# Kernel tuning notes

Hardware: AMD Instinct MI355X
Metric: run time of the kernel (lower is better)

Reference implementation:

```python
import jax, jax.numpy as jnp
import numpy as np

N = 3000          # num_sample (nodes)
N_OMICS = 3000    # input feature dims for both omics
ENC1, ENC2, NZ = 256, 128, 64


def _xavier(key, fan_in, fan_out):
    limit = float(np.sqrt(6.0 / (fan_in + fan_out)))
    return jax.random.uniform(key, (fan_in, fan_out), jnp.float32, -limit, limit)


def setup_inputs() -> dict:
    key = jax.random.key(0)
    ks = jax.random.split(key, 20)
    inp = {
        "omics_1": jax.random.normal(ks[0], (N, N_OMICS), jnp.float32),
        "omics_2": jax.random.normal(ks[1], (N, N_OMICS), jnp.float32),
    }
    # random dense adjacency, row-normalized (as a typical normalized graph operator)
    for i, name in enumerate(["adj_feature_omics1", "adj_feature_omics2",
                              "adj_spatial_omics1", "adj_spatial_omics2"]):
        a = jax.random.uniform(ks[2 + i], (N, N), jnp.float32)
        inp[name] = a / jnp.sum(a, axis=1, keepdims=True)
    # GNNLayer weights for the four GAE encoders (xavier uniform, as in reset_parameters)
    dims = [(N_OMICS, ENC1), (ENC1, ENC2), (ENC2, NZ)]
    kidx = 6
    for enc in ["f1", "f2", "s1", "s2"]:
        for li, (fi, fo) in enumerate(dims, start=1):
            inp[f"w_{enc}_{li}"] = _xavier(ks[kidx], fi, fo)
            kidx += 1
    return inp


def _gae_encoder(x, adj, w1, w2, w3):
    # GNNLayer: support = act(x @ W); out = spmm(adj, support). Dropout is identity (eval).
    z = adj @ jnp.tanh(x @ w1)          # [N, ENC1]
    z = adj @ jnp.tanh(z @ w2)          # [N, ENC2]
    z = adj @ (z @ w3)                  # [N, NZ]  (no activation on layer 3)
    adj_hat = jax.nn.sigmoid(z @ z.T)   # [N, N]
    return z, adj_hat


def reference(omics_1, omics_2,
              adj_feature_omics1, adj_feature_omics2,
              adj_spatial_omics1, adj_spatial_omics2,
              w_f1_1, w_f1_2, w_f1_3,
              w_f2_1, w_f2_2, w_f2_3,
              w_s1_1, w_s1_2, w_s1_3,
              w_s2_1, w_s2_2, w_s2_3):
    _, a1 = _gae_encoder(omics_1, adj_feature_omics1, w_f1_1, w_f1_2, w_f1_3)
    _, a2 = _gae_encoder(omics_2, adj_feature_omics2, w_f2_1, w_f2_2, w_f2_3)
    _, a3 = _gae_encoder(omics_1, adj_spatial_omics1, w_s1_1, w_s1_2, w_s1_3)
    _, a4 = _gae_encoder(omics_2, adj_spatial_omics2, w_s2_1, w_s2_2, w_s2_3)
    # stacked reconstructed adjacencies from the four encoders [4, N, N]
    return jnp.stack([a1, a2, a3, a4], axis=0)
```

## Files before the change

### kernel.cpp

```cpp
#include <hip/hip_runtime.h>
#include <stdint.h>
#include <stddef.h>


typedef __attribute__((ext_vector_type(8))) _Float16 half8;
typedef __attribute__((ext_vector_type(4))) float f32x4;

#define PAD 3072
#define MR  3000
#define SQ_STRIDE ((size_t)PAD * PAD)
#define CAST_BLK 1600
#define WT_BLK   128

static __device__ __forceinline__ void async_cp16(const _Float16* g, _Float16* l) {
    __builtin_amdgcn_global_load_lds((const __attribute__((address_space(1))) void*)g,
                                     (__attribute__((address_space(3))) void*)l, 16, 0, 0);
}

struct PrepArgs {
    const float* csrc[6];  _Float16* cdst[6];
    const float* Wsrc[12]; _Float16* Wdst[3];
};

__global__ __launch_bounds__(256) void prep2(PrepArgs p) {
    __shared__ _Float16 lt[64 * 64];
    const int b = blockIdx.x;
    const int t = threadIdx.x;
    if (b < CAST_BLK) {
        const int UPA = PAD * PAD / 8;
        const int TOT = 6 * UPA;
        for (int base = b * 2048; base < TOT; base += CAST_BLK * 2048) {
            f32x4 v[8][2];
            #pragma unroll
            for (int k = 0; k < 8; ++k) {
                const int u   = base + (k << 8) + t;
                const int arr = u / UPA;
                const int rem = u - arr * UPA;
                const int row = rem / 384;
                const int c0  = (rem - row * 384) * 8;
                if (row < MR && c0 < MR) {
                    const float* sp = p.csrc[arr] + (size_t)row * MR + c0;
                    v[k][0] = __builtin_nontemporal_load((const f32x4*)sp);
                    v[k][1] = __builtin_nontemporal_load((const f32x4*)(sp + 4));
                } else {
                    v[k][0] = (f32x4){0.f, 0.f, 0.f, 0.f};
                    v[k][1] = (f32x4){0.f, 0.f, 0.f, 0.f};
                }
            }
            #pragma unroll
            for (int k = 0; k < 8; ++k) {
                const int u   = base + (k << 8) + t;
                const int arr = u / UPA;
                const int rem = u - arr * UPA;
                const int row = rem / 384;
                const int c0  = (rem - row * 384) * 8;
                half8 h;
                #pragma unroll
                for (int j = 0; j < 4; ++j) {
                    h[j]     = (_Float16)v[k][0][j];
                    h[4 + j] = (_Float16)v[k][1][j];
                }
                *(half8*)(p.cdst[arr] + (size_t)row * PAD + c0) = h;
            }
        }
    } else {
        for (int tile = b - CAST_BLK; tile < 816; tile += WT_BLK) {
            const int enc = tile / 204;
            int rem = tile - enc * 204;
            const float* src; _Float16* dst; int fi, fo, ldk, kt, rt;
            if (rem < 192) {
                src = p.Wsrc[enc * 3 + 0]; dst = p.Wdst[0] + (size_t)enc * 256 * PAD;
                fi = MR; fo = 256; ldk = PAD; kt = rem >> 2; rt = rem & 3;
            } else if (rem < 200) {
                rem -= 192;
                src = p.Wsrc[enc * 3 + 1]; dst = p.Wdst[1] + (size_t)enc * 128 * 256;
                fi = 256; fo = 128; ldk = 256; kt = rem >> 1; rt = rem & 1;
            } else {
                rem -= 200;
                src = p.Wsrc[enc * 3 + 2]; dst = p.Wdst[2] + (size_t)enc * 128 * 128;
                fi = 128; fo = 64; ldk = 128; kt = rem >> 1; rt = rem & 1;
            }
            const int k0 = kt * 64, r0 = rt * 64;
            __syncthreads();
            {
                const int kr = t >> 2, cc = (t & 3) << 4;
                const int gk = k0 + kr;
                const bool kok = gk < fi;
                #pragma unroll
                for (int j = 0; j < 16; ++j) {
                    const int gr = r0 + cc + j;
                    const float v = (kok && gr < fo) ? src[(size_t)gk * fo + gr] : 0.f;
                    lt[(cc + j) * 64 + kr] = (_Float16)v;
                }
            }
            __syncthreads();
            {
                const int rr = t >> 2, kk = (t & 3) << 4;
                half8 a  = *(half8*)&lt[rr * 64 + kk];
                half8 bb = *(half8*)&lt[rr * 64 + kk + 8];
                _Float16* dp = dst + (size_t)(r0 + rr) * ldk + k0 + kk;
                *(half8*)dp = a;
                *(half8*)(dp + 8) = bb;
            }
        }
    }
}

struct GArgs {
    const _Float16* Aall; size_t aStride; int aMask;
    const _Float16* Ball; size_t bStride; int bMask;
    void* Call; size_t cStride;
    int M, Ncols, Kp, lda, ldb, ldc, mBound, nBound;
};

template<int ACT, int OMODE, int S>
__global__ __launch_bounds__(256, 3)
void gemm_bt(GArgs ga)
{
    __shared__ _Float16 smem[16384];

    const int z   = blockIdx.z;
    const int e   = z / S;
    const int ksl = z - e * S;
    const int Kslice = ga.Kp / S;
    const int kbase  = ksl * Kslice;

    const _Float16* A = ga.Aall + (size_t)(e & ga.aMask) * ga.aStride;
    const _Float16* B = ga.Ball + (size_t)(e & ga.bMask) * ga.bStride;

    const int tm = blockIdx.x * 128;
    const int tn = blockIdx.y * 128;
    const int t    = threadIdx.x;
    const int lane = t & 63;
    const int w    = t >> 6;
    const int wm   = (w >> 1) * 64;
    const int wn   = (w & 1) * 64;
    const int lr   = lane & 15;
    const int lg   = lane >> 4;

    const int sr  = t >> 2;
    const int sch = t & 3;

    f32x4 acc[4][4];
    const f32x4 zero = {0.f, 0.f, 0.f, 0.f};
    #pragma unroll
    for (int i = 0; i < 4; ++i)
        #pragma unroll
        for (int j = 0; j < 4; ++j) acc[i][j] = zero;

    const int nht = Kslice >> 5;

    auto STAGE = [&](int ht, int buf) {
        const int k0 = kbase + (ht << 5);
        _Float16* As = smem + buf * 8192;
        _Float16* Bs = As + 4096;
        #pragma unroll
        for (int i = 0; i < 2; ++i) {
            const int row = sr + i * 64;
            const int sc  = sch ^ (row & 3);
            async_cp16(A + (size_t)(tm + row) * ga.lda + k0 + sc * 8,
                       As + (row * 4 + sch) * 8);
        }
        #pragma unroll
        for (int i = 0; i < 2; ++i) {
            const int row = sr + i * 64;
            const int sc  = sch ^ (row & 3);
            async_cp16(B + (size_t)(tn + row) * ga.ldb + k0 + sc * 8,
                       Bs + (row * 4 + sch) * 8);
        }
    };

    STAGE(0, 0);
    __syncthreads();
    for (int h = 0; h < nht; ++h) {
        const int cur = h & 1;
        if (h + 1 < nht) STAGE(h + 1, cur ^ 1);
        const _Float16* As = smem + cur * 8192;
        const _Float16* Bs = As + 4096;
        half8 af[4], bf[4];
        #pragma unroll
        for (int mi = 0; mi < 4; ++mi) {
            const int ra = wm + mi * 16 + lr;
            const int ch = lg ^ (ra & 3);
            af[mi] = *(const half8*)(As + ra * 32 + ch * 8);
        }
        #pragma unroll
        for (int ni = 0; ni < 4; ++ni) {
            const int rb = wn + ni * 16 + lr;
            const int ch = lg ^ (rb & 3);
            bf[ni] = *(const half8*)(Bs + rb * 32 + ch * 8);
        }
        #pragma unroll
        for (int mi = 0; mi < 4; ++mi)
            #pragma unroll
            for (int ni = 0; ni < 4; ++ni)
                acc[mi][ni] = __builtin_amdgcn_mfma_f32_16x16x32_f16(
                    af[mi], bf[ni], acc[mi][ni], 0, 0, 0);
        __syncthreads();
    }

    if (OMODE == 0) {
        _Float16* C = (_Float16*)ga.Call + (size_t)e * ga.cStride;
        #pragma unroll
        for (int mi = 0; mi < 4; ++mi)
            #pragma unroll
            for (int rr = 0; rr < 4; ++rr) {
                const int m = tm + wm + mi * 16 + lg * 4 + rr;
                #pragma unroll
                for (int ni = 0; ni < 4; ++ni) {
                    const int n = tn + wn + ni * 16 + lr;
                    float x = acc[mi][ni][rr];
                    if (ACT) x = tanhf(x);
                    const bool ok = (m < ga.M) && (n < ga.Ncols);
                    C[(size_t)m * ga.ldc + n] = ok ? (_Float16)x : (_Float16)0.f;
                }
            }
    } else if (OMODE == 1) {
        _Float16* Cp = (_Float16*)ga.Call + (size_t)z * ga.cStride;
        _Float16* ep = smem + w * 2048;
        #pragma unroll
        for (int hs = 0; hs < 2; ++hs) {
            __syncthreads();
            #pragma unroll
            for (int mi2 = 0; mi2 < 2; ++mi2)
                #pragma unroll
                for (int ni = 0; ni < 4; ++ni)
                    #pragma unroll
                    for (int rr = 0; rr < 4; ++rr) {
                        const int row = mi2 * 16 + lg * 4 + rr;
                        const int col = ni * 16 + lr;
                        const int sw  = (((row ^ (row >> 2)) & 3) << 4);
                        ep[row * 64 + (col ^ sw)] = (_Float16)acc[hs * 2 + mi2][ni][rr];
                    }
            __syncthreads();
            #pragma unroll
            for (int it = 0; it < 4; ++it) {
                const int row = it * 8 + (lane >> 3);
                const int c0  = (lane & 7) * 8;
                const int sw  = (((row ^ (row >> 2)) & 3) << 4);
                half8 v = *(const half8*)&ep[row * 64 + (c0 ^ sw)];
                const int gm = tm + wm + hs * 32 + row;
                const int gn = tn + wn + c0;
                *(half8*)&Cp[(size_t)gm * ga.ldc + gn] = v;
            }
        }
    } else {
        float* Cp = (float*)ga.Call + (size_t)e * ga.cStride;
        float* ep = (float*)smem + w * 2048;
        #pragma unroll
        for (int hs = 0; hs < 2; ++hs) {
            __syncthreads();
            #pragma unroll
            for (int mi2 = 0; mi2 < 2; ++mi2)
                #pragma unroll
                for (int ni = 0; ni < 4; ++ni)
                    #pragma unroll
                    for (int rr = 0; rr < 4; ++rr) {
                        const int row = mi2 * 16 + lg * 4 + rr;
                        const int col = ni * 16 + lr;
                        const int sw  = (((row ^ (row >> 2)) & 3) << 4);
                        ep[row * 64 + (col ^ sw)] = acc[hs * 2 + mi2][ni][rr];
                    }
            __syncthreads();
            #pragma unroll
            for (int r2 = 0; r2 < 8; ++r2) {
                const int row = r2 * 4 + (lane >> 4);
                const int c4  = (lane & 15) * 4;
                const int sw  = (((row ^ (row >> 2)) & 3) << 4);
                f32x4 v = *(const f32x4*)&ep[row * 64 + (c4 ^ sw)];
                const int gm = tm + wm + hs * 32 + row;
                const int gn = tn + wn + c4;
                if (gm < ga.mBound && gn < ga.nBound) {
                    #pragma unroll
                    for (int j = 0; j < 4; ++j)
                        v[j] = 1.0f / (1.0f + __expf(-v[j]));
                    __builtin_nontemporal_store(v, (f32x4*)&Cp[(size_t)gm * ga.ldc + gn]);
                }
            }
        }
    }
}

template<int ACT, int S>
__global__ __launch_bounds__(256)
void reduce_k(const _Float16* __restrict__ P, _Float16* __restrict__ out, size_t region)
{
    const size_t e    = blockIdx.y;
    const size_t base = (size_t)(blockIdx.x * 256 + threadIdx.x) * 8;
    const _Float16* p0 = P + e * S * region + base;
    float s[8] = {0.f, 0.f, 0.f, 0.f, 0.f, 0.f, 0.f, 0.f};
    #pragma unroll
    for (int si = 0; si < S; ++si) {
        half8 v = *(const half8*)(p0 + (size_t)si * region);
        #pragma unroll
        for (int j = 0; j < 8; ++j) s[j] += (float)v[j];
    }
    half8 h;
    #pragma unroll
    for (int j = 0; j < 8; ++j) {
        float x = s[j];
        if (ACT) x = tanhf(x);
        h[j] = (_Float16)x;
    }
    *(half8*)(out + e * region + base) = h;
}

extern "C" void kernel_launch(void* const* d_in, const int* in_sizes, int n_in,
                              void* d_out, int out_size, void* d_ws, size_t ws_size,
                              hipStream_t stream)
{
    const size_t R1 = 786432;
    const size_t R2 = 393216;

    _Float16* Adj    = (_Float16*)d_out;
    _Float16* Part16 = Adj + 4 * SQ_STRIDE;

    _Float16* hb = (_Float16*)d_ws;
    size_t off = 0;
    auto alloc = [&](size_t elems) { _Float16* p = hb + off; off += elems; return p; };
    _Float16* Xh  = alloc(2 * SQ_STRIDE);
    _Float16* T1  = alloc(4 * R1);
    _Float16* Z1  = alloc(4 * R1);
    _Float16* T2  = alloc(4 * R2);
    _Float16* Z2  = alloc(4 * R2);
    _Float16* T3  = alloc(4 * R2);
    _Float16* Z3  = alloc(4 * R2);
    _Float16* W1t = alloc(4ull * 256 * PAD);
    _Float16* W2t = alloc(4ull * 128 * 256);
    _Float16* W3t = alloc(4ull * 128 * 128);

    PrepArgs pa;
    pa.csrc[0] = (const float*)d_in[0]; pa.cdst[0] = Xh;
    pa.csrc[1] = (const float*)d_in[1]; pa.cdst[1] = Xh + SQ_STRIDE;
    for (int i = 0; i < 4; ++i) {
        pa.csrc[2 + i] = (const float*)d_in[2 + i];
        pa.cdst[2 + i] = Adj + (size_t)i * SQ_STRIDE;
    }
    for (int enc = 0; enc < 4; ++enc)
        for (int li = 0; li < 3; ++li)
            pa.Wsrc[enc * 3 + li] = (const float*)d_in[6 + enc * 3 + li];
    pa.Wdst[0] = W1t; pa.Wdst[1] = W2t; pa.Wdst[2] = W3t;
    prep2<<<dim3(CAST_BLK + WT_BLK, 1, 1), 256, 0, stream>>>(pa);

    const int BIG = 1 << 30;

    GArgs g1 = { W1t, (size_t)256 * PAD, 3, Xh, SQ_STRIDE, 1,
                 Part16, R1, 256, PAD, PAD, PAD, PAD, PAD, BIG, BIG };
    gemm_bt<0, 1, 4><<<dim3(2, 24, 16), 256, 0, stream>>>(g1);
    reduce_k<1, 4><<<dim3(384, 4, 1), 256, 0, stream>>>(Part16, T1, R1);

    GArgs g2 = { Adj, SQ_STRIDE, 3, T1, R1, 3,
                 Part16, R1, PAD, 256, PAD, PAD, PAD, 256, BIG, BIG };
    gemm_bt<0, 1, 4><<<dim3(24, 2, 16), 256, 0, stream>>>(g2);
    reduce_k<0, 4><<<dim3(384, 4, 1), 256, 0, stream>>>(Part16, Z1, R1);

    GArgs g3 = { W2t, (size_t)128 * 256, 3, Z1, R1, 3,
                 T2, R2, 128, PAD, 256, 256, 256, PAD, BIG, BIG };
    gemm_bt<1, 0, 1><<<dim3(1, 24, 4), 256, 0, stream>>>(g3);

    GArgs g4 = { Adj, SQ_STRIDE, 3, T2, R2, 3,
                 Part16, R2, PAD, 128, PAD, PAD, PAD, 128, BIG, BIG };
    gemm_bt<0, 1, 8><<<dim3(24, 1, 32), 256, 0, stream>>>(g4);
    reduce_k<0, 8><<<dim3(192, 4, 1), 256, 0, stream>>>(Part16, Z2, R2);

    GArgs g5 = { W3t, (size_t)128 * 128, 3, Z2, R2, 3,
                 T3, R2, 128, PAD, 128, 128, 128, PAD, BIG, BIG };
    gemm_bt<0, 0, 1><<<dim3(1, 24, 4), 256, 0, stream>>>(g5);

    GArgs g6 = { Adj, SQ_STRIDE, 3, T3, R2, 3,
                 Part16, R2, PAD, 128, PAD, PAD, PAD, 128, BIG, BIG };
    gemm_bt<0, 1, 8><<<dim3(24, 1, 32), 256, 0, stream>>>(g6);
    reduce_k<0, 8><<<dim3(192, 4, 1), 256, 0, stream>>>(Part16, Z3, R2);

    GArgs g7 = { Z3, R2, 3, Z3, R2, 3,
                 d_out, (size_t)MR * MR, MR, MR, 64, 128, 128, MR, MR, MR };
    gemm_bt<0, 2, 1><<<dim3(24, 24, 4), 256, 0, stream>>>(g7);
}
```

Before: 265.9 us.

## Replace split-K with partial reductions by smaller-tile full-K GEMMs

Drops split-K for the big GEMMs along with their fp16 partial buffers and separate reduce kernels. Each GEMM now runs over the full K with templated tile shapes (128x64, 64x128, 64x64) to keep enough blocks in the grid. Tanh moves into the GEMM epilogue. This removes the partial-sum write/read traffic and extra launches, but gives fewer blocks and longer K loops per block. It also changes the cast block count and the occupancy hints.

```diff
diff --git a/kernel.cpp b/kernel.cpp
--- a/kernel.cpp
+++ b/kernel.cpp
@@ -9,7 +9,7 @@
 #define PAD 3072
 #define MR  3000
 #define SQ_STRIDE ((size_t)PAD * PAD)
-#define CAST_BLK 1600
+#define CAST_BLK 1728
 #define WT_BLK   128
 
 static __device__ __forceinline__ void async_cp16(const _Float16* g, _Float16* l) {
@@ -113,60 +113,57 @@
     int M, Ncols, Kp, lda, ldb, ldc, mBound, nBound;
 };
 
-template<int ACT, int OMODE, int S>
-__global__ __launch_bounds__(256, 3)
+template<int ACT, int OMODE, int BM, int BN>
+__global__ __launch_bounds__(256, (BM == 128 && BN == 128) ? 2 : 4)
 void gemm_bt(GArgs ga)
 {
-    __shared__ _Float16 smem[16384];
-
-    const int z   = blockIdx.z;
-    const int e   = z / S;
-    const int ksl = z - e * S;
-    const int Kslice = ga.Kp / S;
-    const int kbase  = ksl * Kslice;
-
+    constexpr int AM  = BM / 32;
+    constexpr int AN  = BN / 32;
+    constexpr int AIT = BM / 64;
+    constexpr int BIT = BN / 64;
+    constexpr int HALF = (BM + BN) * 32;
+    __shared__ _Float16 smem[2 * HALF];
+
+    const int e = blockIdx.z;
     const _Float16* A = ga.Aall + (size_t)(e & ga.aMask) * ga.aStride;
     const _Float16* B = ga.Ball + (size_t)(e & ga.bMask) * ga.bStride;
 
-    const int tm = blockIdx.x * 128;
-    const int tn = blockIdx.y * 128;
+    const int tm = blockIdx.x * BM;
+    const int tn = blockIdx.y * BN;
     const int t    = threadIdx.x;
     const int lane = t & 63;
     const int w    = t >> 6;
-    const int wm   = (w >> 1) * 64;
-    const int wn   = (w & 1) * 64;
+    const int wm   = (w >> 1) * (BM / 2);
+    const int wn   = (w & 1) * (BN / 2);
     const int lr   = lane & 15;
     const int lg   = lane >> 4;
 
-    const int sr  = t >> 2;
-    const int sch = t & 3;
-
-    f32x4 acc[4][4];
+    f32x4 acc[AM][AN];
     const f32x4 zero = {0.f, 0.f, 0.f, 0.f};
     #pragma unroll
-    for (int i = 0; i < 4; ++i)
-        #pragma unroll
-        for (int j = 0; j < 4; ++j) acc[i][j] = zero;
-
-    const int nht = Kslice >> 5;
+    for (int i = 0; i < AM; ++i)
+        #pragma unroll
+        for (int j = 0; j < AN; ++j) acc[i][j] = zero;
+
+    const int nht = ga.Kp >> 5;
 
     auto STAGE = [&](int ht, int buf) {
-        const int k0 = kbase + (ht << 5);
-        _Float16* As = smem + buf * 8192;
-        _Float16* Bs = As + 4096;
-        #pragma unroll
-        for (int i = 0; i < 2; ++i) {
-            const int row = sr + i * 64;
+        const int k0 = ht << 5;
+        _Float16* As = smem + buf * HALF;
+        _Float16* Bs = As + BM * 32;
+        #pragma unroll
+        for (int i = 0; i < AIT; ++i) {
+            const int c = t + i * 256;
+            const int row = c >> 2, sch = c & 3;
             const int sc  = sch ^ (row & 3);
-            async_cp16(A + (size_t)(tm + row) * ga.lda + k0 + sc * 8,
-                       As + (row * 4 + sch) * 8);
-        }
-        #pragma unroll
-        for (int i = 0; i < 2; ++i) {
-            const int row = sr + i * 64;
+            async_cp16(A + (size_t)(tm + row) * ga.lda + k0 + sc * 8, As + c * 8);
+        }
+        #pragma unroll
+        for (int i = 0; i < BIT; ++i) {
+            const int c = t + i * 256;
+            const int row = c >> 2, sch = c & 3;
             const int sc  = sch ^ (row & 3);
-            async_cp16(B + (size_t)(tn + row) * ga.ldb + k0 + sc * 8,
-                       Bs + (row * 4 + sch) * 8);
+            async_cp16(B + (size_t)(tn + row) * ga.ldb + k0 + sc * 8, Bs + c * 8);
         }
     };
 
@@ -175,25 +172,25 @@
     for (int h = 0; h < nht; ++h) {
         const int cur = h & 1;
         if (h + 1 < nht) STAGE(h + 1, cur ^ 1);
-        const _Float16* As = smem + cur * 8192;
-        const _Float16* Bs = As + 4096;
-        half8 af[4], bf[4];
-        #pragma unroll
-        for (int mi = 0; mi < 4; ++mi) {
+        const _Float16* As = smem + cur * HALF;
+        const _Float16* Bs = As + BM * 32;
+        half8 af[AM], bf[AN];
+        #pragma unroll
+        for (int mi = 0; mi < AM; ++mi) {
             const int ra = wm + mi * 16 + lr;
             const int ch = lg ^ (ra & 3);
             af[mi] = *(const half8*)(As + ra * 32 + ch * 8);
         }
         #pragma unroll
-        for (int ni = 0; ni < 4; ++ni) {
+        for (int ni = 0; ni < AN; ++ni) {
             const int rb = wn + ni * 16 + lr;
             const int ch = lg ^ (rb & 3);
             bf[ni] = *(const half8*)(Bs + rb * 32 + ch * 8);
         }
         #pragma unroll
-        for (int mi = 0; mi < 4; ++mi)
-            #pragma unroll
-            for (int ni = 0; ni < 4; ++ni)
+        for (int mi = 0; mi < AM; ++mi)
+            #pragma unroll
+            for (int ni = 0; ni < AN; ++ni)
                 acc[mi][ni] = __builtin_amdgcn_mfma_f32_16x16x32_f16(
                     af[mi], bf[ni], acc[mi][ni], 0, 0, 0);
         __syncthreads();
@@ -202,12 +199,12 @@
     if (OMODE == 0) {
         _Float16* C = (_Float16*)ga.Call + (size_t)e * ga.cStride;
         #pragma unroll
-        for (int mi = 0; mi < 4; ++mi)
+        for (int mi = 0; mi < AM; ++mi)
             #pragma unroll
             for (int rr = 0; rr < 4; ++rr) {
                 const int m = tm + wm + mi * 16 + lg * 4 + rr;
                 #pragma unroll
-                for (int ni = 0; ni < 4; ++ni) {
+                for (int ni = 0; ni < AN; ++ni) {
                     const int n = tn + wn + ni * 16 + lr;
                     float x = acc[mi][ni][rr];
                     if (ACT) x = tanhf(x);
@@ -215,36 +212,8 @@
                     C[(size_t)m * ga.ldc + n] = ok ? (_Float16)x : (_Float16)0.f;
                 }
             }
-    } else if (OMODE == 1) {
-        _Float16* Cp = (_Float16*)ga.Call + (size_t)z * ga.cStride;
-        _Float16* ep = smem + w * 2048;
-        #pragma unroll
-        for (int hs = 0; hs < 2; ++hs) {
-            __syncthreads();
-            #pragma unroll
-            for (int mi2 = 0; mi2 < 2; ++mi2)
-                #pragma unroll
-                for (int ni = 0; ni < 4; ++ni)
-                    #pragma unroll
-                    for (int rr = 0; rr < 4; ++rr) {
-                        const int row = mi2 * 16 + lg * 4 + rr;
-                        const int col = ni * 16 + lr;
-                        const int sw  = (((row ^ (row >> 2)) & 3) << 4);
-                        ep[row * 64 + (col ^ sw)] = (_Float16)acc[hs * 2 + mi2][ni][rr];
-                    }
-            __syncthreads();
-            #pragma unroll
-            for (int it = 0; it < 4; ++it) {
-                const int row = it * 8 + (lane >> 3);
-                const int c0  = (lane & 7) * 8;
-                const int sw  = (((row ^ (row >> 2)) & 3) << 4);
-                half8 v = *(const half8*)&ep[row * 64 + (c0 ^ sw)];
-                const int gm = tm + wm + hs * 32 + row;
-                const int gn = tn + wn + c0;
-                *(half8*)&Cp[(size_t)gm * ga.ldc + gn] = v;
-            }
-        }
     } else {
+        static_assert(OMODE != 2 || (BM == 128 && BN == 128), "OMODE2 is 128x128");
         float* Cp = (float*)ga.Call + (size_t)e * ga.cStride;
         float* ep = (float*)smem + w * 2048;
         #pragma unroll
@@ -281,30 +250,6 @@
     }
 }
 
-template<int ACT, int S>
-__global__ __launch_bounds__(256)
-void reduce_k(const _Float16* __restrict__ P, _Float16* __restrict__ out, size_t region)
-{
-    const size_t e    = blockIdx.y;
-    const size_t base = (size_t)(blockIdx.x * 256 + threadIdx.x) * 8;
-    const _Float16* p0 = P + e * S * region + base;
-    float s[8] = {0.f, 0.f, 0.f, 0.f, 0.f, 0.f, 0.f, 0.f};
-    #pragma unroll
-    for (int si = 0; si < S; ++si) {
-        half8 v = *(const half8*)(p0 + (size_t)si * region);
-        #pragma unroll
-        for (int j = 0; j < 8; ++j) s[j] += (float)v[j];
-    }
-    half8 h;
-    #pragma unroll
-    for (int j = 0; j < 8; ++j) {
-        float x = s[j];
-        if (ACT) x = tanhf(x);
-        h[j] = (_Float16)x;
-    }
-    *(half8*)(out + e * region + base) = h;
-}
-
 extern "C" void kernel_launch(void* const* d_in, const int* in_sizes, int n_in,
                               void* d_out, int out_size, void* d_ws, size_t ws_size,
                               hipStream_t stream)
@@ -312,8 +257,7 @@
     const size_t R1 = 786432;
     const size_t R2 = 393216;
 
-    _Float16* Adj    = (_Float16*)d_out;
-    _Float16* Part16 = Adj + 4 * SQ_STRIDE;
+    _Float16* Adj = (_Float16*)d_out;
 
     _Float16* hb = (_Float16*)d_ws;
     size_t off = 0;
@@ -345,34 +289,30 @@
     const int BIG = 1 << 30;
 
     GArgs g1 = { W1t, (size_t)256 * PAD, 3, Xh, SQ_STRIDE, 1,
-                 Part16, R1, 256, PAD, PAD, PAD, PAD, PAD, BIG, BIG };
-    gemm_bt<0, 1, 4><<<dim3(2, 24, 16), 256, 0, stream>>>(g1);
-    reduce_k<1, 4><<<dim3(384, 4, 1), 256, 0, stream>>>(Part16, T1, R1);
+                 T1, R1, 256, PAD, PAD, PAD, PAD, PAD, BIG, BIG };
+    gemm_bt<1, 0, 128, 64><<<dim3(2, 48, 4), 256, 0, stream>>>(g1);
 
     GArgs g2 = { Adj, SQ_STRIDE, 3, T1, R1, 3,
-                 Part16, R1, PAD, 256, PAD, PAD, PAD, 256, BIG, BIG };
-    gemm_bt<0, 1, 4><<<dim3(24, 2, 16), 256, 0, stream>>>(g2);
-    reduce_k<0, 4><<<dim3(384, 4, 1), 256, 0, stream>>>(Part16, Z1, R1);
+                 Z1, R1, PAD, 256, PAD, PAD, PAD, 256, BIG, BIG };
+    gemm_bt<0, 0, 64, 128><<<dim3(48, 2, 4), 256, 0, stream>>>(g2);
 
     GArgs g3 = { W2t, (size_t)128 * 256, 3, Z1, R1, 3,
                  T2, R2, 128, PAD, 256, 256, 256, PAD, BIG, BIG };
-    gemm_bt<1, 0, 1><<<dim3(1, 24, 4), 256, 0, stream>>>(g3);
+    gemm_bt<1, 0, 128, 64><<<dim3(1, 48, 4), 256, 0, stream>>>(g3);
 
     GArgs g4 = { Adj, SQ_STRIDE, 3, T2, R2, 3,
-                 Part16, R2, PAD, 128, PAD, PAD, PAD, 128, BIG, BIG };
-    gemm_bt<0, 1, 8><<<dim3(24, 1, 32), 256, 0, stream>>>(g4);
-    reduce_k<0, 8><<<dim3(192, 4, 1), 256, 0, stream>>>(Part16, Z2, R2);
+                 Z2, R2, PAD, 128, PAD, PAD, PAD, 128, BIG, BIG };
+    gemm_bt<0, 0, 64, 64><<<dim3(48, 2, 4), 256, 0, stream>>>(g4);
 
     GArgs g5 = { W3t, (size_t)128 * 128, 3, Z2, R2, 3,
                  T3, R2, 128, PAD, 128, 128, 128, PAD, BIG, BIG };
-    gemm_bt<0, 0, 1><<<dim3(1, 24, 4), 256, 0, stream>>>(g5);
+    gemm_bt<0, 0, 128, 64><<<dim3(1, 48, 4), 256, 0, stream>>>(g5);
 
     GArgs g6 = { Adj, SQ_STRIDE, 3, T3, R2, 3,
-                 Part16, R2, PAD, 128, PAD, PAD, PAD, 128, BIG, BIG };
-    gemm_bt<0, 1, 8><<<dim3(24, 1, 32), 256, 0, stream>>>(g6);
-    reduce_k<0, 8><<<dim3(192, 4, 1), 256, 0, stream>>>(Part16, Z3, R2);
+                 Z3, R2, PAD, 128, PAD, PAD, PAD, 128, BIG, BIG };
+    gemm_bt<0, 0, 64, 64><<<dim3(48, 2, 4), 256, 0, stream>>>(g6);
 
     GArgs g7 = { Z3, R2, 3, Z3, R2, 3,
                  d_out, (size_t)MR * MR, MR, MR, 64, 128, 128, MR, MR, MR };
-    gemm_bt<0, 2, 1><<<dim3(24, 24, 4), 256, 0, stream>>>(g7);
+    gemm_bt<0, 2, 128, 128><<<dim3(24, 24, 4), 256, 0, stream>>>(g7);
 }
```

Result: slower. 300.6 us (+13.1%).

## Overlap adjacency fp32-to-fp16 cast with first-layer GEMM main loop

Applied to the files above, without the earlier changes.

Moves the conversion of the four adjacency matrices out of the prep kernel and into the layer-1 X·W1 GEMM. Each K-iteration of that GEMM loads one 8-element chunk of adjacency and stores it as fp16 on the next iteration, so the cast's memory traffic overlaps the GEMM's compute. The prep kernel now only casts the two omics inputs, with fewer blocks. This adds register pressure and extra global traffic inside the GEMM, and it relies on the grid size times iterations exactly covering the four adjacency arrays.

```diff
diff --git a/kernel.cpp b/kernel.cpp
--- a/kernel.cpp
+++ b/kernel.cpp
@@ -9,7 +9,8 @@
 #define PAD 3072
 #define MR  3000
 #define SQ_STRIDE ((size_t)PAD * PAD)
-#define CAST_BLK 1600
+#define UPA (PAD * PAD / 8)
+#define CAST_BLK 576
 #define WT_BLK   128
 
 static __device__ __forceinline__ void async_cp16(const _Float16* g, _Float16* l) {
@@ -18,7 +19,7 @@
 }
 
 struct PrepArgs {
-    const float* csrc[6];  _Float16* cdst[6];
+    const float* csrc[2];  _Float16* cdst[2];
     const float* Wsrc[12]; _Float16* Wdst[3];
 };
 
@@ -27,8 +28,7 @@
     const int b = blockIdx.x;
     const int t = threadIdx.x;
     if (b < CAST_BLK) {
-        const int UPA = PAD * PAD / 8;
-        const int TOT = 6 * UPA;
+        const int TOT = 2 * UPA;
         for (int base = b * 2048; base < TOT; base += CAST_BLK * 2048) {
             f32x4 v[8][2];
             #pragma unroll
@@ -112,10 +112,11 @@
     void* Call; size_t cStride;
     int M, Ncols, Kp, lda, ldb, ldc, mBound, nBound;
 };
-
-template<int ACT, int OMODE, int S>
+struct CastA { const float* src[4]; _Float16* dst; };
+
+template<int ACT, int OMODE, int S, int CAST>
 __global__ __launch_bounds__(256, 3)
-void gemm_bt(GArgs ga)
+void gemm_bt(GArgs ga, CastA ca)
 {
     __shared__ _Float16 smem[16384];
 
@@ -150,6 +151,10 @@
 
     const int nht = Kslice >> 5;
 
+    const int fid = blockIdx.x + gridDim.x * (blockIdx.y + gridDim.y * blockIdx.z);
+    f32x4 cv0, cv1;
+    _Float16* cdp = nullptr;
+
     auto STAGE = [&](int ht, int buf) {
         const int k0 = kbase + (ht << 5);
         _Float16* As = smem + buf * 8192;
@@ -175,6 +180,30 @@
     for (int h = 0; h < nht; ++h) {
         const int cur = h & 1;
         if (h + 1 < nht) STAGE(h + 1, cur ^ 1);
+        if (CAST) {
+            if (h > 0) {
+                half8 hh;
+                #pragma unroll
+                for (int j = 0; j < 4; ++j) {
+                    hh[j] = (_Float16)cv0[j]; hh[4 + j] = (_Float16)cv1[j];
+                }
+                *(half8*)cdp = hh;
+            }
+            const int g    = (fid * nht + h) * 256 + t;
+            const int arr  = g / UPA;
+            const int rem  = g - arr * UPA;
+            const int crow = rem / 384;
+            const int cc0  = (rem - crow * 384) * 8;
+            cdp = ca.dst + (size_t)arr * SQ_STRIDE + (size_t)crow * PAD + cc0;
+            if (crow < MR && cc0 < MR) {
+                const float* sp = ca.src[arr] + (size_t)crow * MR + cc0;
+                cv0 = __builtin_nontemporal_load((const f32x4*)sp);
+                cv1 = __builtin_nontemporal_load((const f32x4*)(sp + 4));
+            } else {
+                cv0 = (f32x4){0.f, 0.f, 0.f, 0.f};
+                cv1 = (f32x4){0.f, 0.f, 0.f, 0.f};
+            }
+        }
         const _Float16* As = smem + cur * 8192;
         const _Float16* Bs = As + 4096;
         half8 af[4], bf[4];
@@ -197,6 +226,14 @@
                 acc[mi][ni] = __builtin_amdgcn_mfma_f32_16x16x32_f16(
                     af[mi], bf[ni], acc[mi][ni], 0, 0, 0);
         __syncthreads();
+    }
+    if (CAST) {
+        half8 hh;
+        #pragma unroll
+        for (int j = 0; j < 4; ++j) {
+            hh[j] = (_Float16)cv0[j]; hh[4 + j] = (_Float16)cv1[j];
+        }
+        *(half8*)cdp = hh;
     }
 
     if (OMODE == 0) {
@@ -241,7 +278,7 @@
                 half8 v = *(const half8*)&ep[row * 64 + (c0 ^ sw)];
                 const int gm = tm + wm + hs * 32 + row;
                 const int gn = tn + wn + c0;
-                *(half8*)&Cp[(size_t)gm * ga.ldc + gn] = v;
+                *(half8*)&((_Float16*)Cp)[(size_t)gm * ga.ldc + gn] = v;
             }
         }
     } else {
@@ -332,10 +369,6 @@
     PrepArgs pa;
     pa.csrc[0] = (const float*)d_in[0]; pa.cdst[0] = Xh;
     pa.csrc[1] = (const float*)d_in[1]; pa.cdst[1] = Xh + SQ_STRIDE;
-    for (int i = 0; i < 4; ++i) {
-        pa.csrc[2 + i] = (const float*)d_in[2 + i];
-        pa.cdst[2 + i] = Adj + (size_t)i * SQ_STRIDE;
-    }
     for (int enc = 0; enc < 4; ++enc)
         for (int li = 0; li < 3; ++li)
             pa.Wsrc[enc * 3 + li] = (const float*)d_in[6 + enc * 3 + li];
@@ -343,36 +376,40 @@
     prep2<<<dim3(CAST_BLK + WT_BLK, 1, 1), 256, 0, stream>>>(pa);
 
     const int BIG = 1 << 30;
+    CastA cnone = { { nullptr, nullptr, nullptr, nullptr }, nullptr };
 
     GArgs g1 = { W1t, (size_t)256 * PAD, 3, Xh, SQ_STRIDE, 1,
                  Part16, R1, 256, PAD, PAD, PAD, PAD, PAD, BIG, BIG };
-    gemm_bt<0, 1, 4><<<dim3(2, 24, 16), 256, 0, stream>>>(g1);
+    CastA ca;
+    for (int i = 0; i < 4; ++i) ca.src[i] = (const float*)d_in[2 + i];
+    ca.dst = Adj;
+    gemm_bt<0, 1, 4, 1><<<dim3(2, 24, 16), 256, 0, stream>>>(g1, ca);
     reduce_k<1, 4><<<dim3(384, 4, 1), 256, 0, stream>>>(Part16, T1, R1);
 
     GArgs g2 = { Adj, SQ_STRIDE, 3, T1, R1, 3,
                  Part16, R1, PAD, 256, PAD, PAD, PAD, 256, BIG, BIG };
-    gemm_bt<0, 1, 4><<<dim3(24, 2, 16), 256, 0, stream>>>(g2);
+    gemm_bt<0, 1, 4, 0><<<dim3(24, 2, 16), 256, 0, stream>>>(g2, cnone);
     reduce_k<0, 4><<<dim3(384, 4, 1), 256, 0, stream>>>(Part16, Z1, R1);
 
     GArgs g3 = { W2t, (size_t)128 * 256, 3, Z1, R1, 3,
                  T2, R2, 128, PAD, 256, 256, 256, PAD, BIG, BIG };
-    gemm_bt<1, 0, 1><<<dim3(1, 24, 4), 256, 0, stream>>>(g3);
+    gemm_bt<1, 0, 1, 0><<<dim3(1, 24, 4), 256, 0, stream>>>(g3, cnone);
 
     GArgs g4 = { Adj, SQ_STRIDE, 3, T2, R2, 3,
                  Part16, R2, PAD, 128, PAD, PAD, PAD, 128, BIG, BIG };
-    gemm_bt<0, 1, 8><<<dim3(24, 1, 32), 256, 0, stream>>>(g4);
+    gemm_bt<0, 1, 8, 0><<<dim3(24, 1, 32), 256, 0, stream>>>(g4, cnone);
     reduce_k<0, 8><<<dim3(192, 4, 1), 256, 0, stream>>>(Part16, Z2, R2);
 
     GArgs g5 = { W3t, (size_t)128 * 128, 3, Z2, R2, 3,
                  T3, R2, 128, PAD, 128, 128, 128, PAD, BIG, BIG };
-    gemm_bt<0, 0, 1><<<dim3(1, 24, 4), 256, 0, stream>>>(g5);
+    gemm_bt<0, 0, 1, 0><<<dim3(1, 24, 4), 256, 0, stream>>>(g5, cnone);
 
     GArgs g6 = { Adj, SQ_STRIDE, 3, T3, R2, 3,
                  Part16, R2, PAD, 128, PAD, PAD, PAD, 128, BIG, BIG };
-    gemm_bt<0, 1, 8><<<dim3(24, 1, 32), 256, 0, stream>>>(g6);
+    gemm_bt<0, 1, 8, 0><<<dim3(24, 1, 32), 256, 0, stream>>>(g6, cnone);
     reduce_k<0, 8><<<dim3(192, 4, 1), 256, 0, stream>>>(Part16, Z3, R2);
 
     GArgs g7 = { Z3, R2, 3, Z3, R2, 3,
                  d_out, (size_t)MR * MR, MR, MR, 64, 128, 128, MR, MR, MR };
-    gemm_bt<0, 2, 1><<<dim3(24, 24, 4), 256, 0, stream>>>(g7);
+    gemm_bt<0, 2, 1, 0><<<dim3(24, 24, 4), 256, 0, stream>>>(g7, cnone);
 }
```

Result: faster. 258.7 us (median of 2 runs) (-2.7%).

## Read fp32 adjacency directly in GEMMs instead of pre-casting to fp16

Applied to the files above, without the earlier changes.

Drops the prep pass that cast the four fp32 adjacency matrices to padded fp16. The three adjacency GEMMs now load fp32 tiles straight into LDS and convert to fp16 in registers before the MFMA. This removes a full read and write of four 3000x3000 matrices. In exchange, each adjacency GEMM reads twice the bytes for A (three times over), uses more LDS, and handles the K tail unpadded, reading past column 3000 of the unpadded rows.

```diff
diff --git a/kernel.cpp b/kernel.cpp
--- a/kernel.cpp
+++ b/kernel.cpp
@@ -9,16 +9,17 @@
 #define PAD 3072
 #define MR  3000
 #define SQ_STRIDE ((size_t)PAD * PAD)
-#define CAST_BLK 1600
+#define UPA (PAD * PAD / 8)
+#define CAST_BLK 576
 #define WT_BLK   128
 
-static __device__ __forceinline__ void async_cp16(const _Float16* g, _Float16* l) {
+static __device__ __forceinline__ void async_cp16(const void* g, void* l) {
     __builtin_amdgcn_global_load_lds((const __attribute__((address_space(1))) void*)g,
                                      (__attribute__((address_space(3))) void*)l, 16, 0, 0);
 }
 
 struct PrepArgs {
-    const float* csrc[6];  _Float16* cdst[6];
+    const float* csrc[2];  _Float16* cdst[2];
     const float* Wsrc[12]; _Float16* Wdst[3];
 };
 
@@ -27,8 +28,7 @@
     const int b = blockIdx.x;
     const int t = threadIdx.x;
     if (b < CAST_BLK) {
-        const int UPA = PAD * PAD / 8;
-        const int TOT = 6 * UPA;
+        const int TOT = 2 * UPA;
         for (int base = b * 2048; base < TOT; base += CAST_BLK * 2048) {
             f32x4 v[8][2];
             #pragma unroll
@@ -109,15 +109,19 @@
 struct GArgs {
     const _Float16* Aall; size_t aStride; int aMask;
     const _Float16* Ball; size_t bStride; int bMask;
+    const float* F32[4];
     void* Call; size_t cStride;
     int M, Ncols, Kp, lda, ldb, ldc, mBound, nBound;
 };
 
-template<int ACT, int OMODE, int S>
+template<int ACT, int OMODE, int S, int AF32>
 __global__ __launch_bounds__(256, 3)
 void gemm_bt(GArgs ga)
 {
-    __shared__ _Float16 smem[16384];
+    constexpr int SMEM_H   = AF32 ? 24576 : 16384;
+    constexpr int BUF_H    = AF32 ? 12288 : 8192;
+    constexpr int B_OFF_H  = AF32 ? 8192  : 4096;
+    __shared__ _Float16 smem[SMEM_H];
 
     const int z   = blockIdx.z;
     const int e   = z / S;
@@ -127,6 +131,7 @@
 
     const _Float16* A = ga.Aall + (size_t)(e & ga.aMask) * ga.aStride;
     const _Float16* B = ga.Ball + (size_t)(e & ga.bMask) * ga.bStride;
+    const float*    Af = AF32 ? ga.F32[e] : nullptr;
 
     const int tm = blockIdx.x * 128;
     const int tn = blockIdx.y * 128;
@@ -152,14 +157,27 @@
 
     auto STAGE = [&](int ht, int buf) {
         const int k0 = kbase + (ht << 5);
-        _Float16* As = smem + buf * 8192;
-        _Float16* Bs = As + 4096;
-        #pragma unroll
-        for (int i = 0; i < 2; ++i) {
-            const int row = sr + i * 64;
-            const int sc  = sch ^ (row & 3);
-            async_cp16(A + (size_t)(tm + row) * ga.lda + k0 + sc * 8,
-                       As + (row * 4 + sch) * 8);
+        _Float16* Ab = smem + buf * BUF_H;
+        _Float16* Bs = Ab + B_OFF_H;
+        if (AF32) {
+            float* As32 = (float*)Ab;
+            #pragma unroll
+            for (int i = 0; i < 4; ++i) {
+                const int c   = t + i * 256;
+                const int row = c >> 3, ch = c & 7;
+                const int pr = ch >> 1, sb = ch & 1;
+                const int sp = ((pr ^ (row & 3)) << 1) + sb;
+                int grow = tm + row; if (grow >= MR) grow = MR - 1;
+                async_cp16(Af + (size_t)grow * MR + k0 + sp * 4, As32 + c * 4);
+            }
+        } else {
+            #pragma unroll
+            for (int i = 0; i < 2; ++i) {
+                const int row = sr + i * 64;
+                const int sc  = sch ^ (row & 3);
+                async_cp16(A + (size_t)(tm + row) * ga.lda + k0 + sc * 8,
+                           Ab + (row * 4 + sch) * 8);
+            }
         }
         #pragma unroll
         for (int i = 0; i < 2; ++i) {
@@ -175,14 +193,32 @@
     for (int h = 0; h < nht; ++h) {
         const int cur = h & 1;
         if (h + 1 < nht) STAGE(h + 1, cur ^ 1);
-        const _Float16* As = smem + cur * 8192;
-        const _Float16* Bs = As + 4096;
+        const _Float16* Ab = smem + cur * BUF_H;
+        const _Float16* Bs = Ab + B_OFF_H;
         half8 af[4], bf[4];
-        #pragma unroll
-        for (int mi = 0; mi < 4; ++mi) {
-            const int ra = wm + mi * 16 + lr;
-            const int ch = lg ^ (ra & 3);
-            af[mi] = *(const half8*)(As + ra * 32 + ch * 8);
+        if (AF32) {
+            const float* As32 = (const float*)Ab;
+            #pragma unroll
+            for (int mi = 0; mi < 4; ++mi) {
+                const int ra = wm + mi * 16 + lr;
+                const int p  = lg ^ (ra & 3);
+                f32x4 lo = *(const f32x4*)(As32 + ra * 32 + p * 8);
+                f32x4 hi = *(const f32x4*)(As32 + ra * 32 + p * 8 + 4);
+                half8 hh;
+                #pragma unroll
+                for (int j = 0; j < 4; ++j) {
+                    hh[j]     = (_Float16)lo[j];
+                    hh[4 + j] = (_Float16)hi[j];
+                }
+                af[mi] = hh;
+            }
+        } else {
+            #pragma unroll
+            for (int mi = 0; mi < 4; ++mi) {
+                const int ra = wm + mi * 16 + lr;
+                const int ch = lg ^ (ra & 3);
+                af[mi] = *(const half8*)(Ab + ra * 32 + ch * 8);
+            }
         }
         #pragma unroll
         for (int ni = 0; ni < 4; ++ni) {
@@ -312,8 +348,7 @@
     const size_t R1 = 786432;
     const size_t R2 = 393216;
 
-    _Float16* Adj    = (_Float16*)d_out;
-    _Float16* Part16 = Adj + 4 * SQ_STRIDE;
+    _Float16* Part16 = (_Float16*)d_out;
 
     _Float16* hb = (_Float16*)d_ws;
     size_t off = 0;
@@ -332,10 +367,6 @@
     PrepArgs pa;
     pa.csrc[0] = (const float*)d_in[0]; pa.cdst[0] = Xh;
     pa.csrc[1] = (const float*)d_in[1]; pa.cdst[1] = Xh + SQ_STRIDE;
-    for (int i = 0; i < 4; ++i) {
-        pa.csrc[2 + i] = (const float*)d_in[2 + i];
-        pa.cdst[2 + i] = Adj + (size_t)i * SQ_STRIDE;
-    }
     for (int enc = 0; enc < 4; ++enc)
         for (int li = 0; li < 3; ++li)
             pa.Wsrc[enc * 3 + li] = (const float*)d_in[6 + enc * 3 + li];
@@ -343,36 +374,45 @@
     prep2<<<dim3(CAST_BLK + WT_BLK, 1, 1), 256, 0, stream>>>(pa);
 
     const int BIG = 1 << 30;
+    const float* AdjF[4] = { (const float*)d_in[2], (const float*)d_in[3],
+                             (const float*)d_in[4], (const float*)d_in[5] };
 
     GArgs g1 = { W1t, (size_t)256 * PAD, 3, Xh, SQ_STRIDE, 1,
+                 { nullptr, nullptr, nullptr, nullptr },
                  Part16, R1, 256, PAD, PAD, PAD, PAD, PAD, BIG, BIG };
-    gemm_bt<0, 1, 4><<<dim3(2, 24, 16), 256, 0, stream>>>(g1);
+    gemm_bt<0, 1, 4, 0><<<dim3(2, 24, 16), 256, 0, stream>>>(g1);
     reduce_k<1, 4><<<dim3(384, 4, 1), 256, 0, stream>>>(Part16, T1, R1);
 
-    GArgs g2 = { Adj, SQ_STRIDE, 3, T1, R1, 3,
-                 Part16, R1, PAD, 256, PAD, PAD, PAD, 256, BIG, BIG };
-    gemm_bt<0, 1, 4><<<dim3(24, 2, 16), 256, 0, stream>>>(g2);
+    GArgs g2 = { nullptr, 0, 0, T1, R1, 3,
+                 { AdjF[0], AdjF[1], AdjF[2], AdjF[3] },
+                 Part16, R1, PAD, 256, PAD, MR, PAD, 256, BIG, BIG };
+    gemm_bt<0, 1, 4, 1><<<dim3(24, 2, 16), 256, 0, stream>>>(g2);
     reduce_k<0, 4><<<dim3(384, 4, 1), 256, 0, stream>>>(Part16, Z1, R1);
 
     GArgs g3 = { W2t, (size_t)128 * 256, 3, Z1, R1, 3,
-                 T2, R2, 128, PAD, 256, 256, 256, PAD, BIG, BIG };
-    gemm_bt<1, 0, 1><<<dim3(1, 24, 4), 256, 0, stream>>>(g3);
-
-    GArgs g4 = { Adj, SQ_STRIDE, 3, T2, R2, 3,
-                 Part16, R2, PAD, 128, PAD, PAD, PAD, 128, BIG, BIG };
-    gemm_bt<0, 1, 8><<<dim3(24, 1, 32), 256, 0, stream>>>(g4);
+                 { nullptr, nullptr, nullptr, nullptr },
+                 T2, R2, 128, MR, 256, 256, 256, PAD, BIG, BIG };
+    gemm_bt<1, 0, 1, 0><<<dim3(1, 24, 4), 256, 0, stream>>>(g3);
+
+    GArgs g4 = { nullptr, 0, 0, T2, R2, 3,
+                 { AdjF[0], AdjF[1], AdjF[2], AdjF[3] },
+                 Part16, R2, PAD, 128, PAD, MR, PAD, 128, BIG, BIG };
+    gemm_bt<0, 1, 8, 1><<<dim3(24, 1, 32), 256, 0, stream>>>(g4);
     reduce_k<0, 8><<<dim3(192, 4, 1), 256, 0, stream>>>(Part16, Z2, R2);
 
     GArgs g5 = { W3t, (size_t)128 * 128, 3, Z2, R2, 3,
-                 T3, R2, 128, PAD, 128, 128, 128, PAD, BIG, BIG };
-    gemm_bt<0, 0, 1><<<dim3(1, 24, 4), 256, 0, stream>>>(g5);
-
-    GArgs g6 = { Adj, SQ_STRIDE, 3, T3, R2, 3,
-                 Part16, R2, PAD, 128, PAD, PAD, PAD, 128, BIG, BIG };
-    gemm_bt<0, 1, 8><<<dim3(24, 1, 32), 256, 0, stream>>>(g6);
+                 { nullptr, nullptr, nullptr, nullptr },
+                 T3, R2, 128, MR, 128, 128, 128, PAD, BIG, BIG };
+    gemm_bt<0, 0, 1, 0><<<dim3(1, 24, 4), 256, 0, stream>>>(g5);
+
+    GArgs g6 = { nullptr, 0, 0, T3, R2, 3,
+                 { AdjF[0], AdjF[1], AdjF[2], AdjF[3] },
+                 Part16, R2, PAD, 128, PAD, MR, PAD, 128, BIG, BIG };
+    gemm_bt<0, 1, 8, 1><<<dim3(24, 1, 32), 256, 0, stream>>>(g6);
     reduce_k<0, 8><<<dim3(192, 4, 1), 256, 0, stream>>>(Part16, Z3, R2);
 
     GArgs g7 = { Z3, R2, 3, Z3, R2, 3,
+                 { nullptr, nullptr, nullptr, nullptr },
                  d_out, (size_t)MR * MR, MR, MR, 64, 128, 128, MR, MR, MR };
-    gemm_bt<0, 2, 1><<<dim3(24, 24, 4), 256, 0, stream>>>(g7);
+    gemm_bt<0, 2, 1, 0><<<dim3(24, 24, 4), 256, 0, stream>>>(g7);
 }
```

After: 275.6 us. 1.04x slower.
